# Kernel optimization log

Measured on AMD Instinct MI355X. Metric: run time of the kernel, lower is better.

## Reference

```python
import jax, jax.numpy as jnp
import numpy as np

DIM = 1024
N_HEAD = 16
HEAD_DIM = DIM // N_HEAD
HIDDEN = 4 * DIM
EPS = 1e-6
NEG = -1e9


def setup_inputs() -> dict:
    key = jax.random.key(0)
    ks = jax.random.split(key, 9)
    B, T = 2, 2048
    x = jax.random.normal(ks[0], (B, T, DIM), dtype=jnp.float32)
    # additive causal mask [T, T]
    mask = jnp.where(jnp.tril(jnp.ones((T, T), dtype=bool)), 0.0, NEG).astype(jnp.float32)
    s = 0.02
    wq = jax.random.normal(ks[1], (DIM, DIM), dtype=jnp.float32) * s
    wk = jax.random.normal(ks[2], (DIM, DIM), dtype=jnp.float32) * s
    wv = jax.random.normal(ks[3], (DIM, DIM), dtype=jnp.float32) * s
    wo = jax.random.normal(ks[4], (DIM, DIM), dtype=jnp.float32) * s
    w1 = jax.random.normal(ks[5], (DIM, HIDDEN), dtype=jnp.float32) * s
    w2 = jax.random.normal(ks[6], (HIDDEN, DIM), dtype=jnp.float32) * s
    g_attn = jnp.ones((DIM,), dtype=jnp.float32)
    g_ffn = jnp.ones((DIM,), dtype=jnp.float32)
    return {"x": x, "mask": mask, "wq": wq, "wk": wk, "wv": wv, "wo": wo,
            "w1": w1, "w2": w2, "g_attn": g_attn, "g_ffn": g_ffn}


def _rmsnorm(x, g):
    norm = jax.lax.rsqrt(jnp.mean(jnp.square(x), axis=-1, keepdims=True) + EPS)
    return (x * norm) * g


def _attention(x, mask, wq, wk, wv, wo):
    B, T, C = x.shape
    # project and split heads: [B, H, T, D]
    q = (x @ wq).reshape(B, T, N_HEAD, HEAD_DIM).transpose(0, 2, 1, 3)
    k = (x @ wk).reshape(B, T, N_HEAD, HEAD_DIM).transpose(0, 2, 1, 3)
    v = (x @ wv).reshape(B, T, N_HEAD, HEAD_DIM).transpose(0, 2, 1, 3)
    attn = jnp.einsum('bhtd,bhsd->bhts', q, k) / np.sqrt(HEAD_DIM).astype(np.float32)
    attn = attn + mask  # broadcast [T,T] over [B,H,T,T]
    p = jax.nn.softmax(attn, axis=-1)
    out = jnp.einsum('bhts,bhsd->bhtd', p, v)
    out = out.transpose(0, 2, 1, 3).reshape(B, T, C)
    return out @ wo


def reference(x, mask, wq, wk, wv, wo, w1, w2, g_attn, g_ffn):
    x = x + _attention(_rmsnorm(x, g_attn), mask, wq, wk, wv, wo)
    h = _rmsnorm(x, g_ffn)
    return x + (jax.nn.silu(h @ w1) @ w2)
```

## Files before the change

### kernel.cpp

```cpp
#include <hip/hip_runtime.h>
#include <hip/hip_bf16.h>
#include <cstdint>
#include <cstddef>

#define DIM    1024
#define NHEAD  16
#define HDIM   64
#define HIDDEN 4096
#define TSEQ   2048
#define TOKENS 4096

typedef __attribute__((ext_vector_type(4))) float  f32x4;
typedef __attribute__((ext_vector_type(8))) short  short8;
typedef __attribute__((ext_vector_type(8))) __bf16 bf16x8;

__device__ __forceinline__ short f2bf(float f) {
    union { float f; uint32_t u; } v; v.f = f;
    uint32_t u = v.u;
    uint32_t r = (u + 0x7fffu + ((u >> 16) & 1u)) >> 16;
    return (short)r;
}

__device__ __forceinline__ f32x4 mfma_bf16(short8 a, short8 b, f32x4 c) {
    return __builtin_amdgcn_mfma_f32_16x16x32_bf16(
        __builtin_bit_cast(bf16x8, a), __builtin_bit_cast(bf16x8, b), c, 0, 0, 0);
}

__global__ __launch_bounds__(256) void transpose_w(
    const float* __restrict__ W, short* __restrict__ Wt, int K, int N)
{
    __shared__ float tile[64][65];
    const int tid = threadIdx.x;
    const int n0 = blockIdx.x * 64, k0 = blockIdx.y * 64;
    for (int i = tid; i < 4096; i += 256) {
        int r = i >> 6, c = i & 63;
        tile[r][c] = W[(size_t)(k0 + r) * N + n0 + c];
    }
    __syncthreads();
    for (int i = tid; i < 4096; i += 256) {
        int r = i >> 6, c = i & 63;
        Wt[(size_t)(n0 + r) * K + k0 + c] = f2bf(tile[c][r]);
    }
}

__global__ __launch_bounds__(256) void transpose_v(
    const short* __restrict__ qkv, short* __restrict__ Vt)
{
    __shared__ short tile[64][72];
    const int tid = threadIdx.x;
    const int s0 = blockIdx.x * 64, bh = blockIdx.y;
    const int b = bh >> 4, h = bh & 15;
    const short* src = qkv + ((size_t)(b * TSEQ + s0)) * 3072 + 2048 + h * 64;
    for (int i = tid; i < 512; i += 256) {
        int r = i >> 3, cg = i & 7;
        *(short8*)&tile[r][cg * 8] = *(const short8*)(src + (size_t)r * 3072 + cg * 8);
    }
    __syncthreads();
    short* dst = Vt + ((size_t)bh * 64) * TSEQ + s0;
    for (int i = tid; i < 512; i += 256) {
        int d = i >> 3, sg = i & 7;
        short8 o;
#pragma unroll
        for (int j = 0; j < 8; ++j) o[j] = tile[sg * 8 + j][d];
        *(short8*)(dst + (size_t)d * TSEQ + sg * 8) = o;
    }
}

__global__ __launch_bounds__(256) void rmsnorm_k(
    const float* __restrict__ x, const float* __restrict__ g, short* __restrict__ out)
{
    const int t = blockIdx.x, tid = threadIdx.x;
    const int wave = tid >> 6, lane = tid & 63;
    const float4 v = ((const float4*)(x + (size_t)t * DIM))[tid];
    float ss = v.x * v.x + v.y * v.y + v.z * v.z + v.w * v.w;
#pragma unroll
    for (int d = 1; d < 64; d <<= 1) ss += __shfl_xor(ss, d, 64);
    __shared__ float red[4];
    if (lane == 0) red[wave] = ss;
    __syncthreads();
    float tot = red[0] + red[1] + red[2] + red[3];
    float rn = rsqrtf(tot * (1.0f / (float)DIM) + 1e-6f);
    const float4 gv = ((const float4*)g)[tid];
    short4 ov = make_short4(f2bf(v.x * rn * gv.x), f2bf(v.y * rn * gv.y),
                            f2bf(v.z * rn * gv.z), f2bf(v.w * rn * gv.w));
    ((short4*)(out + (size_t)t * DIM))[tid] = ov;
}

template <int EPI>
__global__ __launch_bounds__(256) void gemm_bt(
    const short* __restrict__ A, const short* __restrict__ Bt,
    void* __restrict__ Cout, const float* __restrict__ res,
    int M, int N, int K)
{
    __shared__ short As[2][128 * 32];
    __shared__ short Bs[2][128 * 32];
    const int tid  = threadIdx.x;
    const int wave = tid >> 6, lane = tid & 63;
    const int lm = lane & 15, quad = lane >> 4;
    const int wm = wave & 1, wn = wave >> 1;
    const int m0 = blockIdx.y * 128, n0 = blockIdx.x * 128;
    const int Ksl = K / gridDim.z;
    const int kbeg = blockIdx.z * Ksl;
    const int nIter = Ksl >> 5;

    const f32x4 zero = {0.f, 0.f, 0.f, 0.f};
    f32x4 acc[4][4];
#pragma unroll
    for (int i = 0; i < 4; ++i)
#pragma unroll
        for (int j = 0; j < 4; ++j) acc[i][j] = zero;

    const int lrow = wave * 32 + (lane >> 2);
    const int lcol = (lane & 3) * 8;
    const short* Ap = A + (size_t)(m0 + lrow) * K + kbeg + lcol;
    const short* Bp = Bt + (size_t)(n0 + lrow) * K + kbeg + lcol;
    const int woff = lrow * 32 + lcol;

    short8 ga0, ga1, gb0, gb1;
    ga0 = *(const short8*)Ap;
    ga1 = *(const short8*)(Ap + (size_t)16 * K);
    gb0 = *(const short8*)Bp;
    gb1 = *(const short8*)(Bp + (size_t)16 * K);
    Ap += 32; Bp += 32;
    *(short8*)&As[0][woff] = ga0;
    *(short8*)&As[0][woff + 512] = ga1;
    *(short8*)&Bs[0][woff] = gb0;
    *(short8*)&Bs[0][woff + 512] = gb1;
    if (nIter > 1) {
        ga0 = *(const short8*)Ap;
        ga1 = *(const short8*)(Ap + (size_t)16 * K);
        gb0 = *(const short8*)Bp;
        gb1 = *(const short8*)(Bp + (size_t)16 * K);
        Ap += 32; Bp += 32;
    }
    __syncthreads();

    for (int it = 0; it < nIter; ++it) {
        const int cur = it & 1;
        const short* as = As[cur];
        const short* bs = Bs[cur];
        short8 af[4], bf[4];
#pragma unroll
        for (int mt = 0; mt < 4; ++mt)
            af[mt] = *(const short8*)&as[(wm * 64 + mt * 16 + lm) * 32 + quad * 8];
#pragma unroll
        for (int nt = 0; nt < 4; ++nt)
            bf[nt] = *(const short8*)&bs[(wn * 64 + nt * 16 + lm) * 32 + quad * 8];
#pragma unroll
        for (int mt = 0; mt < 4; ++mt)
#pragma unroll
            for (int nt = 0; nt < 4; ++nt)
                acc[mt][nt] = mfma_bf16(af[mt], bf[nt], acc[mt][nt]);

        if (it + 1 < nIter) {
            const int nxt = cur ^ 1;
            *(short8*)&As[nxt][woff] = ga0;
            *(short8*)&As[nxt][woff + 512] = ga1;
            *(short8*)&Bs[nxt][woff] = gb0;
            *(short8*)&Bs[nxt][woff + 512] = gb1;
            if (it + 2 < nIter) {
                ga0 = *(const short8*)Ap;
                ga1 = *(const short8*)(Ap + (size_t)16 * K);
                gb0 = *(const short8*)Bp;
                gb1 = *(const short8*)(Bp + (size_t)16 * K);
                Ap += 32; Bp += 32;
            }
        }
        __syncthreads();
    }

#pragma unroll
    for (int mt = 0; mt < 4; ++mt) {
#pragma unroll
        for (int r = 0; r < 4; ++r) {
            const int row = m0 + wm * 64 + mt * 16 + quad * 4 + r;
#pragma unroll
            for (int nt = 0; nt < 4; ++nt) {
                const int col = n0 + wn * 64 + nt * 16 + lm;
                const size_t idx = (size_t)row * N + col;
                const float v = acc[mt][nt][r];
                if constexpr (EPI == 0) {
                    ((short*)Cout)[idx] = f2bf(v);
                } else if constexpr (EPI == 1) {
                    ((float*)Cout)[idx] = res[idx] + v;
                } else if constexpr (EPI == 2) {
                    ((short*)Cout)[idx] = f2bf(v / (1.0f + __expf(-v)));
                } else {
                    ((float*)Cout)[(size_t)blockIdx.z * M * N + idx] = v;
                }
            }
        }
    }
}

__global__ __launch_bounds__(256) void combine_k(
    const float* __restrict__ p, const float* __restrict__ res,
    float* __restrict__ out, int n)
{
    const int i = blockIdx.x * 256 + threadIdx.x;
    if (i * 4 < n) {
        float4 a = ((const float4*)res)[i];
        float4 b = ((const float4*)p)[i];
        float4 c = ((const float4*)(p + n))[i];
        float4 o = make_float4(a.x + b.x + c.x, a.y + b.y + c.y,
                               a.z + b.z + c.z, a.w + b.w + c.w);
        ((float4*)out)[i] = o;
    }
}

__global__ __launch_bounds__(256) void combine_rms(
    const float* __restrict__ p, const float* __restrict__ res,
    const float* __restrict__ g, float* __restrict__ x2out,
    short* __restrict__ nout)
{
    const int t = blockIdx.x, tid = threadIdx.x;
    const int wave = tid >> 6, lane = tid & 63;
    const size_t base = (size_t)t * DIM / 4;
    float4 a = ((const float4*)res)[base + tid];
    float4 b = ((const float4*)p)[base + tid];
    float4 c = ((const float4*)p)[(size_t)TOKENS * DIM / 4 + base + tid];
    float4 v = make_float4(a.x + b.x + c.x, a.y + b.y + c.y,
                           a.z + b.z + c.z, a.w + b.w + c.w);
    ((float4*)x2out)[base + tid] = v;
    float ss = v.x * v.x + v.y * v.y + v.z * v.z + v.w * v.w;
#pragma unroll
    for (int d = 1; d < 64; d <<= 1) ss += __shfl_xor(ss, d, 64);
    __shared__ float red[4];
    if (lane == 0) red[wave] = ss;
    __syncthreads();
    float tot = red[0] + red[1] + red[2] + red[3];
    float rn = rsqrtf(tot * (1.0f / (float)DIM) + 1e-6f);
    const float4 gv = ((const float4*)g)[tid];
    short4 ov = make_short4(f2bf(v.x * rn * gv.x), f2bf(v.y * rn * gv.y),
                            f2bf(v.z * rn * gv.z), f2bf(v.w * rn * gv.w));
    ((short4*)nout)[base + tid] = ov;
}

#define LP 72
__global__ __launch_bounds__(128) void attn_k(
    const short* __restrict__ qkv, const short* __restrict__ Vt,
    short* __restrict__ out)
{
    __shared__ short Qs[64 * LP];
    __shared__ short Ks[64 * LP];
    __shared__ short Vts[64 * LP];
    __shared__ short Ps[2][32 * LP];

    const int tid = threadIdx.x, wave = tid >> 6, lane = tid & 63;
    const int lm = lane & 15, quad = lane >> 4;
    const int bh = blockIdx.x;
    const int qt = (gridDim.y - 1) - blockIdx.y;
    const int b = bh >> 4, h = bh & 15;
    const int q0 = qt * 64;

    const int rr = tid >> 3, cg = tid & 7;

    const short* qbase = qkv + ((size_t)(b * TSEQ + q0)) * 3072 + h * 64;
#pragma unroll
    for (int j = 0; j < 4; ++j)
        *(short8*)&Qs[(rr + j * 16) * LP + cg * 8] =
            *(const short8*)(qbase + (size_t)(rr + j * 16) * 3072 + cg * 8);

    const short* kb  = qkv + (size_t)b * TSEQ * 3072 + 1024 + h * 64;
    const short* vtb = Vt + (size_t)bh * 64 * TSEQ;

    short8 kr[4], vr[4];
#pragma unroll
    for (int j = 0; j < 4; ++j) {
        kr[j] = *(const short8*)(kb + (size_t)(rr + j * 16) * 3072 + cg * 8);
        vr[j] = *(const short8*)(vtb + (size_t)(rr + j * 16) * TSEQ + cg * 8);
    }

    const f32x4 zero = {0.f, 0.f, 0.f, 0.f};
    f32x4 o_acc[2][4];
#pragma unroll
    for (int mt = 0; mt < 2; ++mt)
#pragma unroll
        for (int t = 0; t < 4; ++t) o_acc[mt][t] = zero;
    float lsum[2][4] = {{0.f, 0.f, 0.f, 0.f}, {0.f, 0.f, 0.f, 0.f}};

    for (int st = 0; st <= qt; ++st) {
        __syncthreads();
#pragma unroll
        for (int j = 0; j < 4; ++j) {
            *(short8*)&Ks[(rr + j * 16) * LP + cg * 8] = kr[j];
            *(short8*)&Vts[(rr + j * 16) * LP + cg * 8] = vr[j];
        }
        __syncthreads();
        if (st < qt) {
            const size_t sn = (size_t)(st + 1) * 64;
#pragma unroll
            for (int j = 0; j < 4; ++j) {
                kr[j] = *(const short8*)(kb + (sn + rr + j * 16) * 3072 + cg * 8);
                vr[j] = *(const short8*)(vtb + (size_t)(rr + j * 16) * TSEQ + sn + cg * 8);
            }
        }

        f32x4 sa[2][4];
#pragma unroll
        for (int mt = 0; mt < 2; ++mt)
#pragma unroll
            for (int nt = 0; nt < 4; ++nt) sa[mt][nt] = zero;
#pragma unroll
        for (int kk = 0; kk < 2; ++kk) {
            short8 aq0 = *(const short8*)&Qs[(wave * 32 + lm) * LP + kk * 32 + quad * 8];
            short8 aq1 = *(const short8*)&Qs[(wave * 32 + 16 + lm) * LP + kk * 32 + quad * 8];
#pragma unroll
            for (int nt = 0; nt < 4; ++nt) {
                short8 bk = *(const short8*)&Ks[(nt * 16 + lm) * LP + kk * 32 + quad * 8];
                sa[0][nt] = mfma_bf16(aq0, bk, sa[0][nt]);
                sa[1][nt] = mfma_bf16(aq1, bk, sa[1][nt]);
            }
        }

        const int s0 = st * 64;
        const bool band = (st == qt);
#pragma unroll
        for (int mt = 0; mt < 2; ++mt) {
            const int qrow = q0 + wave * 32 + mt * 16 + quad * 4;
#pragma unroll
            for (int nt = 0; nt < 4; ++nt) {
                const int col = s0 + nt * 16 + lm;
#pragma unroll
                for (int r = 0; r < 4; ++r) {
                    float p = __expf(0.125f * sa[mt][nt][r]);
                    if (band && col > qrow + r) p = 0.f;
                    lsum[mt][r] += p;
                    Ps[wave][(mt * 16 + quad * 4 + r) * LP + nt * 16 + lm] =
                        (short)(__builtin_bit_cast(uint32_t, p) >> 16);
                }
            }
        }

#pragma unroll
        for (int kk = 0; kk < 2; ++kk) {
            short8 ap0 = *(const short8*)&Ps[wave][lm * LP + kk * 32 + quad * 8];
            short8 ap1 = *(const short8*)&Ps[wave][(16 + lm) * LP + kk * 32 + quad * 8];
#pragma unroll
            for (int t = 0; t < 4; ++t) {
                short8 bv = *(const short8*)&Vts[(t * 16 + lm) * LP + kk * 32 + quad * 8];
                o_acc[0][t] = mfma_bf16(ap0, bv, o_acc[0][t]);
                o_acc[1][t] = mfma_bf16(ap1, bv, o_acc[1][t]);
            }
        }
    }

#pragma unroll
    for (int mt = 0; mt < 2; ++mt)
#pragma unroll
        for (int r = 0; r < 4; ++r) {
            float s = lsum[mt][r];
#pragma unroll
            for (int d = 1; d < 16; d <<= 1) s += __shfl_xor(s, d, 16);
            lsum[mt][r] = s;
        }

#pragma unroll
    for (int mt = 0; mt < 2; ++mt)
#pragma unroll
        for (int r = 0; r < 4; ++r) {
            const float inv = 1.0f / lsum[mt][r];
            const int token = b * TSEQ + q0 + wave * 32 + mt * 16 + quad * 4 + r;
#pragma unroll
            for (int t = 0; t < 4; ++t)
                out[(size_t)token * 1024 + h * 64 + t * 16 + lm] = f2bf(o_acc[mt][t][r] * inv);
        }
}

extern "C" void kernel_launch(void* const* d_in, const int* in_sizes, int n_in,
                              void* d_out, int out_size, void* d_ws, size_t ws_size,
                              hipStream_t stream)
{
    const float* x      = (const float*)d_in[0];
    const float* wq     = (const float*)d_in[2];
    const float* wk     = (const float*)d_in[3];
    const float* wv     = (const float*)d_in[4];
    const float* wo     = (const float*)d_in[5];
    const float* w1     = (const float*)d_in[6];
    const float* w2     = (const float*)d_in[7];
    const float* g_attn = (const float*)d_in[8];
    const float* g_ffn  = (const float*)d_in[9];
    float* out = (float*)d_out;

    char* ws = (char*)d_ws;
    const size_t MB = 1024 * 1024;
    short* Wqkv_t = (short*)(ws + 0);
    short* Wo_t   = (short*)(ws + 6 * MB);
    short* W1_t   = (short*)(ws + 8 * MB);
    short* xn     = (short*)(ws + 16 * MB);
    short* hbuf   = (short*)(ws + 24 * MB);
    short* qkv    = (short*)(ws + 32 * MB);
    float* pbufO  = (float*)(ws + 32 * MB);
    short* Vt     = (short*)(ws + 64 * MB);
    float* x2     = (float*)(ws + 64 * MB);
    short* W2_t   = (short*)(ws + 80 * MB);
    float* pbuf2  = (float*)(ws + 0);

    dim3 blk(256);

    transpose_w<<<dim3(16, 16), blk, 0, stream>>>(wq, Wqkv_t, 1024, 1024);
    transpose_w<<<dim3(16, 16), blk, 0, stream>>>(wk, Wqkv_t + (size_t)1024 * 1024, 1024, 1024);
    transpose_w<<<dim3(16, 16), blk, 0, stream>>>(wv, Wqkv_t + (size_t)2048 * 1024, 1024, 1024);
    transpose_w<<<dim3(16, 16), blk, 0, stream>>>(wo, Wo_t, 1024, 1024);
    transpose_w<<<dim3(64, 16), blk, 0, stream>>>(w1, W1_t, 1024, 4096);
    transpose_w<<<dim3(16, 64), blk, 0, stream>>>(w2, W2_t, 4096, 1024);

    rmsnorm_k<<<TOKENS, blk, 0, stream>>>(x, g_attn, xn);

    gemm_bt<0><<<dim3(3072 / 128, TOKENS / 128), blk, 0, stream>>>(
        xn, Wqkv_t, qkv, nullptr, TOKENS, 3072, 1024);

    transpose_v<<<dim3(TSEQ / 64, 32), blk, 0, stream>>>(qkv, Vt);

    attn_k<<<dim3(32, TSEQ / 64), dim3(128), 0, stream>>>(qkv, Vt, xn);

    gemm_bt<3><<<dim3(1024 / 128, TOKENS / 128, 2), blk, 0, stream>>>(
        xn, Wo_t, pbufO, nullptr, TOKENS, 1024, 1024);

    combine_rms<<<TOKENS, blk, 0, stream>>>(pbufO, x, g_ffn, x2, hbuf);

    gemm_bt<2><<<dim3(HIDDEN / 128, TOKENS / 128), blk, 0, stream>>>(
        hbuf, W1_t, qkv, nullptr, TOKENS, HIDDEN, 1024);

    gemm_bt<3><<<dim3(1024 / 128, TOKENS / 128, 2), blk, 0, stream>>>(
        qkv, W2_t, pbuf2, nullptr, TOKENS, 1024, HIDDEN);

    combine_k<<<dim3(TOKENS * DIM / 4 / 256), blk, 0, stream>>>(
        pbuf2, x2, out, TOKENS * DIM);
}
```

Baseline: 394.8 us.

## Deepen GEMM prefetch to two register stages with lightweight LDS barrier

Restructures the bf16 GEMM main loop into a 2x unrolled ping-pong with two sets of prefetch registers, so global loads for the tile two steps ahead are issued before the MFMA work on the current tile. It also replaces __syncthreads with an inline asm barrier that waits only on LDS counters (lgkmcnt), not on outstanding global loads. The aim is to hide global memory latency behind more compute. The cost is more live registers, which may lower occupancy, and the custom barrier relies on correct ordering of the LDS writes.

```diff
diff --git a/kernel.cpp b/kernel.cpp
--- a/kernel.cpp
+++ b/kernel.cpp
@@ -24,6 +24,10 @@
 __device__ __forceinline__ f32x4 mfma_bf16(short8 a, short8 b, f32x4 c) {
     return __builtin_amdgcn_mfma_f32_16x16x32_bf16(
         __builtin_bit_cast(bf16x8, a), __builtin_bit_cast(bf16x8, b), c, 0, 0, 0);
+}
+
+__device__ __forceinline__ void barrier_lds() {
+    asm volatile("s_waitcnt lgkmcnt(0)\n\ts_barrier" ::: "memory");
 }
 
 __global__ __launch_bounds__(256) void transpose_w(
@@ -116,29 +120,10 @@
     const short* Bp = Bt + (size_t)(n0 + lrow) * K + kbeg + lcol;
     const int woff = lrow * 32 + lcol;
 
-    short8 ga0, ga1, gb0, gb1;
-    ga0 = *(const short8*)Ap;
-    ga1 = *(const short8*)(Ap + (size_t)16 * K);
-    gb0 = *(const short8*)Bp;
-    gb1 = *(const short8*)(Bp + (size_t)16 * K);
-    Ap += 32; Bp += 32;
-    *(short8*)&As[0][woff] = ga0;
-    *(short8*)&As[0][woff + 512] = ga1;
-    *(short8*)&Bs[0][woff] = gb0;
-    *(short8*)&Bs[0][woff + 512] = gb1;
-    if (nIter > 1) {
-        ga0 = *(const short8*)Ap;
-        ga1 = *(const short8*)(Ap + (size_t)16 * K);
-        gb0 = *(const short8*)Bp;
-        gb1 = *(const short8*)(Bp + (size_t)16 * K);
-        Ap += 32; Bp += 32;
-    }
-    __syncthreads();
-
-    for (int it = 0; it < nIter; ++it) {
-        const int cur = it & 1;
-        const short* as = As[cur];
-        const short* bs = Bs[cur];
+    short8 a00, a01, b00, b01;
+    short8 a10, a11, b10, b11;
+
+    auto compute = [&](const short* as, const short* bs) {
         short8 af[4], bf[4];
 #pragma unroll
         for (int mt = 0; mt < 4; ++mt)
@@ -151,22 +136,43 @@
 #pragma unroll
             for (int nt = 0; nt < 4; ++nt)
                 acc[mt][nt] = mfma_bf16(af[mt], bf[nt], acc[mt][nt]);
-
+    };
+
+    a00 = *(const short8*)Ap;  a01 = *(const short8*)(Ap + (size_t)16 * K);
+    b00 = *(const short8*)Bp;  b01 = *(const short8*)(Bp + (size_t)16 * K);
+    Ap += 32; Bp += 32;
+    *(short8*)&As[0][woff] = a00;  *(short8*)&As[0][woff + 512] = a01;
+    *(short8*)&Bs[0][woff] = b00;  *(short8*)&Bs[0][woff + 512] = b01;
+    a10 = *(const short8*)Ap;  a11 = *(const short8*)(Ap + (size_t)16 * K);
+    b10 = *(const short8*)Bp;  b11 = *(const short8*)(Bp + (size_t)16 * K);
+    Ap += 32; Bp += 32;
+    barrier_lds();
+
+    for (int it = 0; it < nIter; it += 2) {
+        if (it + 2 < nIter) {
+            a00 = *(const short8*)Ap;  a01 = *(const short8*)(Ap + (size_t)16 * K);
+            b00 = *(const short8*)Bp;  b01 = *(const short8*)(Bp + (size_t)16 * K);
+            Ap += 32; Bp += 32;
+        }
+        compute(As[0], Bs[0]);
         if (it + 1 < nIter) {
-            const int nxt = cur ^ 1;
-            *(short8*)&As[nxt][woff] = ga0;
-            *(short8*)&As[nxt][woff + 512] = ga1;
-            *(short8*)&Bs[nxt][woff] = gb0;
-            *(short8*)&Bs[nxt][woff + 512] = gb1;
+            *(short8*)&As[1][woff] = a10;  *(short8*)&As[1][woff + 512] = a11;
+            *(short8*)&Bs[1][woff] = b10;  *(short8*)&Bs[1][woff + 512] = b11;
+        }
+        barrier_lds();
+        if (it + 1 < nIter) {
+            if (it + 3 < nIter) {
+                a10 = *(const short8*)Ap;  a11 = *(const short8*)(Ap + (size_t)16 * K);
+                b10 = *(const short8*)Bp;  b11 = *(const short8*)(Bp + (size_t)16 * K);
+                Ap += 32; Bp += 32;
+            }
+            compute(As[1], Bs[1]);
             if (it + 2 < nIter) {
-                ga0 = *(const short8*)Ap;
-                ga1 = *(const short8*)(Ap + (size_t)16 * K);
-                gb0 = *(const short8*)Bp;
-                gb1 = *(const short8*)(Bp + (size_t)16 * K);
-                Ap += 32; Bp += 32;
-            }
-        }
-        __syncthreads();
+                *(short8*)&As[0][woff] = a00;  *(short8*)&As[0][woff + 512] = a01;
+                *(short8*)&Bs[0][woff] = b00;  *(short8*)&Bs[0][woff + 512] = b01;
+            }
+            barrier_lds();
+        }
     }
 
 #pragma unroll
```

After: 385.2 us. 1.02x faster.

## Use direct global-to-LDS loads in GEMM pipeline and swap grid block order

Applied to the files above, without the earlier changes.

Replaces the register-staged global->LDS copy in the bf16 GEMM with global_load_lds DMA-style loads, prefetching two stages ahead and synchronizing with explicit vmcnt waits and barriers. This removes the register round-trip and VGPR pressure of staging tiles. It also swaps the grid mapping so blockIdx.x walks M tiles, changing which blocks share weight tiles in cache. The LDS layout written by global_load_lds must match the per-lane offsets assumed by the fragment reads, and the hand-written waitcnt counts are fragile.

```diff
diff --git a/kernel.cpp b/kernel.cpp
--- a/kernel.cpp
+++ b/kernel.cpp
@@ -24,6 +24,16 @@
 __device__ __forceinline__ f32x4 mfma_bf16(short8 a, short8 b, f32x4 c) {
     return __builtin_amdgcn_mfma_f32_16x16x32_bf16(
         __builtin_bit_cast(bf16x8, a), __builtin_bit_cast(bf16x8, b), c, 0, 0, 0);
+}
+
+__device__ __forceinline__ void ldg_lds16(const void* g, void* l) {
+    __builtin_amdgcn_global_load_lds(
+        (const __attribute__((address_space(1))) void*)g,
+        (__attribute__((address_space(3))) void*)l, 16, 0, 0);
+}
+
+__device__ __forceinline__ void barrier_lds() {
+    asm volatile("s_waitcnt lgkmcnt(0)\n\ts_barrier" ::: "memory");
 }
 
 __global__ __launch_bounds__(256) void transpose_w(
@@ -98,7 +108,7 @@
     const int wave = tid >> 6, lane = tid & 63;
     const int lm = lane & 15, quad = lane >> 4;
     const int wm = wave & 1, wn = wave >> 1;
-    const int m0 = blockIdx.y * 128, n0 = blockIdx.x * 128;
+    const int m0 = blockIdx.x * 128, n0 = blockIdx.y * 128;
     const int Ksl = K / gridDim.z;
     const int kbeg = blockIdx.z * Ksl;
     const int nIter = Ksl >> 5;
@@ -112,31 +122,24 @@
 
     const int lrow = wave * 32 + (lane >> 2);
     const int lcol = (lane & 3) * 8;
-    const short* Ap = A + (size_t)(m0 + lrow) * K + kbeg + lcol;
-    const short* Bp = Bt + (size_t)(n0 + lrow) * K + kbeg + lcol;
-    const int woff = lrow * 32 + lcol;
-
-    short8 ga0, ga1, gb0, gb1;
-    ga0 = *(const short8*)Ap;
-    ga1 = *(const short8*)(Ap + (size_t)16 * K);
-    gb0 = *(const short8*)Bp;
-    gb1 = *(const short8*)(Bp + (size_t)16 * K);
-    Ap += 32; Bp += 32;
-    *(short8*)&As[0][woff] = ga0;
-    *(short8*)&As[0][woff + 512] = ga1;
-    *(short8*)&Bs[0][woff] = gb0;
-    *(short8*)&Bs[0][woff + 512] = gb1;
-    if (nIter > 1) {
-        ga0 = *(const short8*)Ap;
-        ga1 = *(const short8*)(Ap + (size_t)16 * K);
-        gb0 = *(const short8*)Bp;
-        gb1 = *(const short8*)(Bp + (size_t)16 * K);
-        Ap += 32; Bp += 32;
-    }
-    __syncthreads();
+    const short* Apre = A + (size_t)(m0 + lrow) * K + kbeg + lcol;
+    const short* Bpre = Bt + (size_t)(n0 + lrow) * K + kbeg + lcol;
+
+    auto stage = [&](int buf) {
+        ldg_lds16(Apre, &As[buf][(wave * 32) * 32]);
+        ldg_lds16(Apre + (size_t)16 * K, &As[buf][(wave * 32 + 16) * 32]);
+        ldg_lds16(Bpre, &Bs[buf][(wave * 32) * 32]);
+        ldg_lds16(Bpre + (size_t)16 * K, &Bs[buf][(wave * 32 + 16) * 32]);
+        Apre += 32; Bpre += 32;
+    };
+
+    stage(0);
+    stage(1);
 
     for (int it = 0; it < nIter; ++it) {
         const int cur = it & 1;
+        asm volatile("s_waitcnt vmcnt(4)" ::: "memory");
+        asm volatile("s_barrier" ::: "memory");
         const short* as = As[cur];
         const short* bs = Bs[cur];
         short8 af[4], bf[4];
@@ -151,22 +154,8 @@
 #pragma unroll
             for (int nt = 0; nt < 4; ++nt)
                 acc[mt][nt] = mfma_bf16(af[mt], bf[nt], acc[mt][nt]);
-
-        if (it + 1 < nIter) {
-            const int nxt = cur ^ 1;
-            *(short8*)&As[nxt][woff] = ga0;
-            *(short8*)&As[nxt][woff + 512] = ga1;
-            *(short8*)&Bs[nxt][woff] = gb0;
-            *(short8*)&Bs[nxt][woff + 512] = gb1;
-            if (it + 2 < nIter) {
-                ga0 = *(const short8*)Ap;
-                ga1 = *(const short8*)(Ap + (size_t)16 * K);
-                gb0 = *(const short8*)Bp;
-                gb1 = *(const short8*)(Bp + (size_t)16 * K);
-                Ap += 32; Bp += 32;
-            }
-        }
-        __syncthreads();
+        barrier_lds();
+        if (it + 2 < nIter) stage(cur);
     }
 
 #pragma unroll
@@ -407,22 +396,22 @@
 
     rmsnorm_k<<<TOKENS, blk, 0, stream>>>(x, g_attn, xn);
 
-    gemm_bt<0><<<dim3(3072 / 128, TOKENS / 128), blk, 0, stream>>>(
+    gemm_bt<0><<<dim3(TOKENS / 128, 3072 / 128), blk, 0, stream>>>(
         xn, Wqkv_t, qkv, nullptr, TOKENS, 3072, 1024);
 
     transpose_v<<<dim3(TSEQ / 64, 32), blk, 0, stream>>>(qkv, Vt);
 
     attn_k<<<dim3(32, TSEQ / 64), dim3(128), 0, stream>>>(qkv, Vt, xn);
 
-    gemm_bt<3><<<dim3(1024 / 128, TOKENS / 128, 2), blk, 0, stream>>>(
+    gemm_bt<3><<<dim3(TOKENS / 128, 1024 / 128, 2), blk, 0, stream>>>(
         xn, Wo_t, pbufO, nullptr, TOKENS, 1024, 1024);
 
     combine_rms<<<TOKENS, blk, 0, stream>>>(pbufO, x, g_ffn, x2, hbuf);
 
-    gemm_bt<2><<<dim3(HIDDEN / 128, TOKENS / 128), blk, 0, stream>>>(
+    gemm_bt<2><<<dim3(TOKENS / 128, HIDDEN / 128), blk, 0, stream>>>(
         hbuf, W1_t, qkv, nullptr, TOKENS, HIDDEN, 1024);
 
-    gemm_bt<3><<<dim3(1024 / 128, TOKENS / 128, 2), blk, 0, stream>>>(
+    gemm_bt<3><<<dim3(TOKENS / 128, 1024 / 128, 2), blk, 0, stream>>>(
         qkv, W2_t, pbuf2, nullptr, TOKENS, 1024, HIDDEN);
 
     combine_k<<<dim3(TOKENS * DIM / 4 / 256), blk, 0, stream>>>(
```

Result: no change. 397.8 us (+0.8%).
